# Kernel optimization log

Measured on AMD Instinct MI355X. Metric: run time of the kernel, lower is better.

## Reference

```python
import jax, jax.numpy as jnp
import numpy as np

BINS = 256
H = 2048
N = 2_000_000


def _tensor2image(x):
    # standard GAN denorm: [-1,1] -> [0,1]
    return (x + 1.0) * 0.5


def _cdf(vals):
    # torch.histc(bins=256, min=0, max=256): unit-width bins, values in [0,255]
    idx = jnp.clip(jnp.floor(vals), 0, BINS - 1).astype(jnp.int32)
    hist = jnp.zeros((BINS,), jnp.float32).at[idx].add(1.0)
    return jnp.cumsum(hist) / hist.sum()


def _trans_table(ref_cdf, adj_cdf):
    # cal_trans: for i in 1..255, first j in 1..255 with adj[j-1] <= ref[i] <= adj[j]
    i_vals = ref_cdf[1:]  # [255]
    cond = (adj_cdf[:-1][None, :] <= i_vals[:, None]) & (i_vals[:, None] <= adj_cdf[1:][None, :])  # [255,255]
    found = cond.any(axis=1)
    first_j = jnp.argmax(cond, axis=1) + 1
    tab = jnp.where(found, first_j, jnp.arange(1, BINS))  # unmatched entries keep identity
    tab = jnp.concatenate([jnp.zeros((1,), tab.dtype), tab])
    tab = tab.at[BINS - 1].set(BINS - 1)
    return tab.astype(jnp.float32)


def _hist_match(dst_img, ref_img, i0, i1, i2, i3):
    # dst_img, ref_img: [3,H,W]; indices: [N]
    dst_align = dst_img[:, i0, i1]  # [3,N]
    ref_align = ref_img[:, i2, i3]  # [3,N]
    cdf_dst = jax.vmap(_cdf)(dst_align)  # [3,256]
    cdf_ref = jax.vmap(_cdf)(ref_align)  # [3,256]
    tables = jax.vmap(_trans_table)(cdf_dst, cdf_ref)  # [3,256]
    bins = jnp.clip(dst_align, 0, BINS - 1).astype(jnp.int32)  # int() truncation on [0,255]
    new_align = jnp.take_along_axis(tables, bins, axis=1)  # [3,N]
    return dst_img.at[:, i0, i1].set(new_align)


def reference(input_data, target_data, mask_src, mask_tar, index0, index1, index2, index3, ref_data):
    inp = _tensor2image(input_data) * 255.0
    tgt = _tensor2image(target_data) * 255.0
    ref = _tensor2image(ref_data) * 255.0
    h = mask_src.shape[2]
    m_src = jnp.broadcast_to(mask_src, (1, 3, h, h))
    m_tar = jnp.broadcast_to(mask_tar, (1, 3, h, h))
    input_masked = inp * m_src
    target_masked = (tgt * m_tar)[0]  # [3,H,W]
    ref_masked = (ref * m_src)[0]     # [3,H,W]
    i0, i1, i2, i3 = index0[0], index1[0], index2[0], index3[0]
    matched = _hist_match(ref_masked, target_masked, i0, i1, i2, i3)[None]  # [1,3,H,W]
    input_match = jax.lax.stop_gradient(matched) * m_src  # no_grad in original
    return jnp.mean((input_masked - input_match) ** 2)


def setup_inputs() -> dict:
    key = jax.random.key(0)
    ks = jax.random.split(key, 9)
    inp = {
        "input_data": jax.random.uniform(ks[0], (1, 3, H, H), jnp.float32, -1.0, 1.0),
        "target_data": jax.random.uniform(ks[1], (1, 3, H, H), jnp.float32, -1.0, 1.0),
        "mask_src": (jax.random.uniform(ks[2], (1, 1, H, H)) > 0.5).astype(jnp.float32),
        "mask_tar": (jax.random.uniform(ks[3], (1, 1, H, H)) > 0.5).astype(jnp.float32),
        "index0": jax.random.randint(ks[4], (1, N), 0, H, jnp.int32),
        "index1": jax.random.randint(ks[5], (1, N), 0, H, jnp.int32),
        "index2": jax.random.randint(ks[6], (1, N), 0, H, jnp.int32),
        "index3": jax.random.randint(ks[7], (1, N), 0, H, jnp.int32),
        "ref_data": jax.random.uniform(ks[8], (1, 3, H, H), jnp.float32, -1.0, 1.0),
    }
    return inp
```

## Files before the change

kernel.cpp:

```cpp
#include <hip/hip_runtime.h>

#define HDIM 2048
#define HH (HDIM * HDIM)
#define NIDX 2000000
#define BINS 256
#define NCOPY 16
#define TL_BLOCKS 2048

#define PART_OFF     0
#define HIST_OFF     20480
#define BITS_OFF     131072
#define PACKED_D_OFF 1048576
#define PACKED_R_OFF 17825792

__global__ __launch_bounds__(256) void pack_kernel(
    const float* __restrict__ ref, const float* __restrict__ tgt,
    const float* __restrict__ msrc, const float* __restrict__ mtar,
    unsigned* __restrict__ packed_d, unsigned* __restrict__ packed_r,
    unsigned* __restrict__ hist, unsigned* __restrict__ bits)
{
    const int gtid = blockIdx.x * 256 + threadIdx.x;
    const int stride = gridDim.x * 256;

    for (int k = gtid; k < NCOPY * 6 * BINS; k += stride) hist[k] = 0;
    for (int k = gtid; k < HH / 32; k += stride) bits[k] = 0;

    for (int g = gtid; g < HH / 4; g += stride) {
        const int p = g * 4;
        const float4 ms4 = *(const float4*)(msrc + p);
        const float4 mt4 = *(const float4*)(mtar + p);
        const float ms[4] = {ms4.x, ms4.y, ms4.z, ms4.w};
        const float mt[4] = {mt4.x, mt4.y, mt4.z, mt4.w};
        unsigned od[4] = {0, 0, 0, 0}, orr[4] = {0, 0, 0, 0};
#pragma unroll
        for (int c = 0; c < 3; c++) {
            const float4 rv = *(const float4*)(ref + c * HH + p);
            const float4 tv = *(const float4*)(tgt + c * HH + p);
            const float r[4] = {rv.x, rv.y, rv.z, rv.w};
            const float tt[4] = {tv.x, tv.y, tv.z, tv.w};
#pragma unroll
            for (int k = 0; k < 4; k++) {
                const float vd = ((r[k] + 1.0f) * 0.5f) * 255.0f * ms[k];
                const float vr = ((tt[k] + 1.0f) * 0.5f) * 255.0f * mt[k];
                const unsigned bd = (unsigned)(int)fminf(fmaxf(floorf(vd), 0.0f), 255.0f);
                const unsigned br = (unsigned)(int)fminf(fmaxf(floorf(vr), 0.0f), 255.0f);
                od[k]  |= bd << (8 * c);
                orr[k] |= br << (8 * c);
            }
        }
        *(uint4*)(packed_d + p) = make_uint4(od[0], od[1], od[2], od[3]);
        *(uint4*)(packed_r + p) = make_uint4(orr[0], orr[1], orr[2], orr[3]);
    }
}

__global__ __launch_bounds__(256) void hist_kernel(
    const unsigned* __restrict__ packed_d, const unsigned* __restrict__ packed_r,
    const int* __restrict__ i0, const int* __restrict__ i1,
    const int* __restrict__ i2, const int* __restrict__ i3,
    unsigned* __restrict__ hist, unsigned* __restrict__ bits)
{
    __shared__ unsigned lhist[6 * BINS];
    for (int k = threadIdx.x; k < 6 * BINS; k += 256) lhist[k] = 0;
    __syncthreads();

    const int stride = gridDim.x * 256;
    for (int q = blockIdx.x * 256 + threadIdx.x; q < NIDX / 4; q += stride) {
        const int4 a = ((const int4*)i0)[q];
        const int4 b = ((const int4*)i1)[q];
        const int4 c = ((const int4*)i2)[q];
        const int4 d = ((const int4*)i3)[q];
        const int pd[4] = {a.x * HDIM + b.x, a.y * HDIM + b.y, a.z * HDIM + b.z, a.w * HDIM + b.w};
        const int pr[4] = {c.x * HDIM + d.x, c.y * HDIM + d.y, c.z * HDIM + d.z, c.w * HDIM + d.w};
        unsigned wd[4], wr[4];
#pragma unroll
        for (int k = 0; k < 4; k++) wd[k] = packed_d[pd[k]];
#pragma unroll
        for (int k = 0; k < 4; k++) wr[k] = packed_r[pr[k]];
#pragma unroll
        for (int k = 0; k < 4; k++) atomicOr(&bits[pd[k] >> 5], 1u << (pd[k] & 31));
#pragma unroll
        for (int k = 0; k < 4; k++) {
            atomicAdd(&lhist[           ( wd[k]        & 255u)], 1u);
            atomicAdd(&lhist[1 * BINS + ((wd[k] >> 8 ) & 255u)], 1u);
            atomicAdd(&lhist[2 * BINS + ((wd[k] >> 16) & 255u)], 1u);
            atomicAdd(&lhist[3 * BINS + ( wr[k]        & 255u)], 1u);
            atomicAdd(&lhist[4 * BINS + ((wr[k] >> 8 ) & 255u)], 1u);
            atomicAdd(&lhist[5 * BINS + ((wr[k] >> 16) & 255u)], 1u);
        }
    }
    __syncthreads();
    unsigned* h = hist + (blockIdx.x & (NCOPY - 1)) * (6 * BINS);
    for (int k = threadIdx.x; k < 6 * BINS; k += 256) {
        const unsigned v = lhist[k];
        if (v) atomicAdd(&h[k], v);
    }
}

__global__ __launch_bounds__(256) void tabloss_kernel(
    const float* __restrict__ inp, const float* __restrict__ ref,
    const float* __restrict__ msrc, const unsigned* __restrict__ hist,
    const unsigned* __restrict__ bits, double* __restrict__ partials)
{
    __shared__ float    cdf[6 * BINS];
    __shared__ float    tab[3 * BINS];
    __shared__ double   red[256];
    __shared__ unsigned wsum[4];

    const int t    = threadIdx.x;
    const int lane = t & 63;
    const int wid  = t >> 6;

    for (int ch = 0; ch < 6; ch++) {
        unsigned x = 0;
#pragma unroll
        for (int cp = 0; cp < NCOPY; cp++) x += hist[cp * (6 * BINS) + ch * BINS + t];
#pragma unroll
        for (int d = 1; d < 64; d <<= 1) {
            const unsigned y = __shfl_up(x, d, 64);
            if (lane >= d) x += y;
        }
        if (lane == 63) wsum[wid] = x;
        __syncthreads();
        unsigned prefix = 0;
        for (int w = 0; w < wid; w++) prefix += wsum[w];
        x += prefix;
        cdf[ch * BINS + t] = (float)x / 2000000.0f;
        __syncthreads();
    }
    for (int c = 0; c < 3; c++) {
        float o;
        if (t == 0)             o = 0.0f;
        else if (t == BINS - 1) o = 255.0f;
        else {
            const float v = cdf[c * BINS + t];
            const float* arr = cdf + (3 + c) * BINS;
            int lo = 0, hi = 256;
            while (lo < hi) { const int mid = (lo + hi) >> 1; if (arr[mid] < v) lo = mid + 1; else hi = mid; }
            const int J0 = ((lo > 1) ? lo : 1) - 1;
            int lo2 = 0, hi2 = 256;
            while (lo2 < hi2) { const int mid = (lo2 + hi2) >> 1; if (arr[mid] <= v) lo2 = mid + 1; else hi2 = mid; }
            const int J1 = ((lo2 - 1) < 254 ? (lo2 - 1) : 254);
            const bool found = (lo2 >= 1) && (J0 <= J1);
            o = found ? (float)(J0 + 1) : (float)t;
        }
        tab[c * BINS + t] = o;
    }
    __syncthreads();

    double local = 0.0;
    const int stride = gridDim.x * 256;
    for (int g = blockIdx.x * 256 + t; g < HH / 4; g += stride) {
        const int p = g * 4;
        const float4 mv = *(const float4*)(msrc + p);
        const unsigned w = bits[p >> 5] >> (p & 31);
        const float m[4] = {mv.x, mv.y, mv.z, mv.w};
#pragma unroll
        for (int c = 0; c < 3; c++) {
            const float4 rv = *(const float4*)(ref + c * HH + p);
            const float4 iv = *(const float4*)(inp + c * HH + p);
            const float r[4] = {rv.x, rv.y, rv.z, rv.w};
            const float x4[4] = {iv.x, iv.y, iv.z, iv.w};
            float s = 0.0f;
#pragma unroll
            for (int k = 0; k < 4; k++) {
                const float mm = m[k];
                const float refm = ((r[k] + 1.0f) * 0.5f) * 255.0f * mm;
                const float inpm = ((x4[k] + 1.0f) * 0.5f) * 255.0f * mm;
                float matchv;
                if ((w >> k) & 1u) {
                    const int bidx = (int)fminf(fmaxf(refm, 0.0f), 255.0f);
                    matchv = tab[c * BINS + bidx];
                } else {
                    matchv = refm;
                }
                const float dd = inpm - matchv * mm;
                s += dd * dd;
            }
            local += (double)s;
        }
    }
    red[t] = local;
    __syncthreads();
    for (int s2 = 128; s2 > 0; s2 >>= 1) {
        if (t < s2) red[t] += red[t + s2];
        __syncthreads();
    }
    if (t == 0) partials[blockIdx.x] = red[0];
}

__global__ __launch_bounds__(256) void finalize_kernel(
    const double* __restrict__ partials, float* __restrict__ out)
{
    const int t = threadIdx.x;
    double s = 0.0;
    for (int k = t; k < TL_BLOCKS; k += 256) s += partials[k];
    __shared__ double red[256];
    red[t] = s;
    __syncthreads();
    for (int s2 = 128; s2 > 0; s2 >>= 1) {
        if (t < s2) red[t] += red[t + s2];
        __syncthreads();
    }
    if (t == 0) out[0] = (float)(red[0] / (double)(3 * HH));
}

extern "C" void kernel_launch(void* const* d_in, const int* in_sizes, int n_in,
                              void* d_out, int out_size, void* d_ws, size_t ws_size,
                              hipStream_t stream)
{
    const float* input_data  = (const float*)d_in[0];
    const float* target_data = (const float*)d_in[1];
    const float* mask_src    = (const float*)d_in[2];
    const float* mask_tar    = (const float*)d_in[3];
    const int*   i0          = (const int*)d_in[4];
    const int*   i1          = (const int*)d_in[5];
    const int*   i2          = (const int*)d_in[6];
    const int*   i3          = (const int*)d_in[7];
    const float* ref_data    = (const float*)d_in[8];
    float* out = (float*)d_out;

    char* ws = (char*)d_ws;
    double*   partials = (double*)(ws + PART_OFF);
    unsigned* hist     = (unsigned*)(ws + HIST_OFF);
    unsigned* bits     = (unsigned*)(ws + BITS_OFF);
    unsigned* packed_d = (unsigned*)(ws + PACKED_D_OFF);
    unsigned* packed_r = (unsigned*)(ws + PACKED_R_OFF);

    pack_kernel<<<2048, 256, 0, stream>>>(ref_data, target_data, mask_src, mask_tar,
                                          packed_d, packed_r, hist, bits);
    hist_kernel<<<2048, 256, 0, stream>>>(packed_d, packed_r, i0, i1, i2, i3, hist, bits);
    tabloss_kernel<<<TL_BLOCKS, 256, 0, stream>>>(input_data, ref_data, mask_src, hist,
                                                  bits, partials);
    finalize_kernel<<<1, 256, 0, stream>>>(partials, out);
}
```

Before: 338.3 us.

## Bucket gather indices by address slice for L2-local histogram gathers

```diff
diff --git a/kernel.cpp b/kernel.cpp
--- a/kernel.cpp
+++ b/kernel.cpp
@@ -3,53 +3,139 @@
 #define HDIM 2048
 #define HH (HDIM * HDIM)
 #define NIDX 2000000
+#define QUADS (NIDX / 4)
 #define BINS 256
 #define NCOPY 16
 #define TL_BLOCKS 2048
 
+#define PACKB 2048
+#define BBLK 256
+#define QPB ((QUADS + BBLK - 1) / BBLK)
+#define NSLICE 8
+#define CAP 1152
+
 #define PART_OFF     0
 #define HIST_OFF     20480
 #define BITS_OFF     131072
+#define CNTS_OFF     655360
 #define PACKED_D_OFF 1048576
 #define PACKED_R_OFF 17825792
+#define BKT_PD_OFF   34603008
+#define BKT_PR_OFF   44040192
+#define WS_NEED      (BKT_PR_OFF + (size_t)BBLK * NSLICE * CAP * 4)
 
 __global__ __launch_bounds__(256) void pack_kernel(
     const float* __restrict__ ref, const float* __restrict__ tgt,
     const float* __restrict__ msrc, const float* __restrict__ mtar,
+    const int* __restrict__ i0, const int* __restrict__ i1,
+    const int* __restrict__ i2, const int* __restrict__ i3,
     unsigned* __restrict__ packed_d, unsigned* __restrict__ packed_r,
+    unsigned* __restrict__ hist, unsigned* __restrict__ bits,
+    unsigned* __restrict__ bkt_pd, unsigned* __restrict__ bkt_pr,
+    unsigned* __restrict__ cnts)
+{
+    const int t = threadIdx.x;
+    if (blockIdx.x < PACKB) {
+        const int gtid = blockIdx.x * 256 + t;
+        const int stride = PACKB * 256;
+
+        for (int k = gtid; k < NCOPY * 6 * BINS; k += stride) hist[k] = 0;
+        for (int k = gtid; k < HH / 32; k += stride) bits[k] = 0;
+
+        for (int g = gtid; g < HH / 4; g += stride) {
+            const int p = g * 4;
+            const float4 ms4 = *(const float4*)(msrc + p);
+            const float4 mt4 = *(const float4*)(mtar + p);
+            const float ms[4] = {ms4.x, ms4.y, ms4.z, ms4.w};
+            const float mt[4] = {mt4.x, mt4.y, mt4.z, mt4.w};
+            unsigned od[4] = {0, 0, 0, 0}, orr[4] = {0, 0, 0, 0};
+#pragma unroll
+            for (int c = 0; c < 3; c++) {
+                const float4 rv = *(const float4*)(ref + c * HH + p);
+                const float4 tv = *(const float4*)(tgt + c * HH + p);
+                const float r[4] = {rv.x, rv.y, rv.z, rv.w};
+                const float tt[4] = {tv.x, tv.y, tv.z, tv.w};
+#pragma unroll
+                for (int k = 0; k < 4; k++) {
+                    const float vd = ((r[k] + 1.0f) * 0.5f) * 255.0f * ms[k];
+                    const float vr = ((tt[k] + 1.0f) * 0.5f) * 255.0f * mt[k];
+                    const unsigned bd = (unsigned)(int)fminf(fmaxf(floorf(vd), 0.0f), 255.0f);
+                    const unsigned br = (unsigned)(int)fminf(fmaxf(floorf(vr), 0.0f), 255.0f);
+                    od[k]  |= bd << (8 * c);
+                    orr[k] |= br << (8 * c);
+                }
+            }
+            *(uint4*)(packed_d + p) = make_uint4(od[0], od[1], od[2], od[3]);
+            *(uint4*)(packed_r + p) = make_uint4(orr[0], orr[1], orr[2], orr[3]);
+        }
+    } else {
+        __shared__ unsigned lcur[2 * NSLICE];
+        if (t < 2 * NSLICE) lcur[t] = 0;
+        __syncthreads();
+
+        const int bb  = blockIdx.x - PACKB;
+        const int qlo = bb * QPB;
+        const int qhi = (qlo + QPB < QUADS) ? (qlo + QPB) : QUADS;
+        for (int q = qlo + t; q < qhi; q += 256) {
+            const int4 a = ((const int4*)i0)[q];
+            const int4 b = ((const int4*)i1)[q];
+            const int4 c = ((const int4*)i2)[q];
+            const int4 d = ((const int4*)i3)[q];
+            const int pd[4] = {a.x * HDIM + b.x, a.y * HDIM + b.y, a.z * HDIM + b.z, a.w * HDIM + b.w};
+            const int pr[4] = {c.x * HDIM + d.x, c.y * HDIM + d.y, c.z * HDIM + d.z, c.w * HDIM + d.w};
+#pragma unroll
+            for (int k = 0; k < 4; k++) {
+                const int sd = pd[k] >> 19;
+                const unsigned pos = atomicAdd(&lcur[sd], 1u);
+                if (pos < CAP) bkt_pd[(bb * NSLICE + sd) * CAP + pos] = (unsigned)pd[k];
+                const int sr = pr[k] >> 19;
+                const unsigned pos2 = atomicAdd(&lcur[NSLICE + sr], 1u);
+                if (pos2 < CAP) bkt_pr[(bb * NSLICE + sr) * CAP + pos2] = (unsigned)pr[k];
+            }
+        }
+        __syncthreads();
+        if (t < NSLICE) {
+            const unsigned v = lcur[t];
+            cnts[0 * BBLK * NSLICE + bb * NSLICE + t] = (v < CAP) ? v : CAP;
+        } else if (t < 2 * NSLICE) {
+            const unsigned v = lcur[t];
+            cnts[1 * BBLK * NSLICE + bb * NSLICE + (t - NSLICE)] = (v < CAP) ? v : CAP;
+        }
+    }
+}
+
+__global__ __launch_bounds__(256) void hist_bucket_kernel(
+    const unsigned* __restrict__ packed_d, const unsigned* __restrict__ packed_r,
+    const unsigned* __restrict__ bkt_pd, const unsigned* __restrict__ bkt_pr,
+    const unsigned* __restrict__ cnts,
     unsigned* __restrict__ hist, unsigned* __restrict__ bits)
 {
-    const int gtid = blockIdx.x * 256 + threadIdx.x;
-    const int stride = gridDim.x * 256;
-
-    for (int k = gtid; k < NCOPY * 6 * BINS; k += stride) hist[k] = 0;
-    for (int k = gtid; k < HH / 32; k += stride) bits[k] = 0;
-
-    for (int g = gtid; g < HH / 4; g += stride) {
-        const int p = g * 4;
-        const float4 ms4 = *(const float4*)(msrc + p);
-        const float4 mt4 = *(const float4*)(mtar + p);
-        const float ms[4] = {ms4.x, ms4.y, ms4.z, ms4.w};
-        const float mt[4] = {mt4.x, mt4.y, mt4.z, mt4.w};
-        unsigned od[4] = {0, 0, 0, 0}, orr[4] = {0, 0, 0, 0};
-#pragma unroll
-        for (int c = 0; c < 3; c++) {
-            const float4 rv = *(const float4*)(ref + c * HH + p);
-            const float4 tv = *(const float4*)(tgt + c * HH + p);
-            const float r[4] = {rv.x, rv.y, rv.z, rv.w};
-            const float tt[4] = {tv.x, tv.y, tv.z, tv.w};
-#pragma unroll
-            for (int k = 0; k < 4; k++) {
-                const float vd = ((r[k] + 1.0f) * 0.5f) * 255.0f * ms[k];
-                const float vr = ((tt[k] + 1.0f) * 0.5f) * 255.0f * mt[k];
-                const unsigned bd = (unsigned)(int)fminf(fmaxf(floorf(vd), 0.0f), 255.0f);
-                const unsigned br = (unsigned)(int)fminf(fmaxf(floorf(vr), 0.0f), 255.0f);
-                od[k]  |= bd << (8 * c);
-                orr[k] |= br << (8 * c);
-            }
-        }
-        *(uint4*)(packed_d + p) = make_uint4(od[0], od[1], od[2], od[3]);
-        *(uint4*)(packed_r + p) = make_uint4(orr[0], orr[1], orr[2], orr[3]);
+    __shared__ unsigned lhist[6 * BINS];
+    const int t = threadIdx.x;
+    for (int k = t; k < 6 * BINS; k += 256) lhist[k] = 0;
+    __syncthreads();
+
+    const int side = blockIdx.x >> 11;
+    const int s    = blockIdx.x & 7;
+    const int j    = (blockIdx.x & 2047) >> 3;
+    const unsigned cnt = cnts[side * BBLK * NSLICE + j * NSLICE + s];
+    const unsigned* bkt = (side ? bkt_pr : bkt_pd) + (j * NSLICE + s) * CAP;
+    const unsigned* packed = side ? packed_r : packed_d;
+    const int hbase = side ? 3 * BINS : 0;
+
+    for (unsigned i = t; i < cnt; i += 256) {
+        const unsigned p = bkt[i];
+        const unsigned w = packed[p];
+        if (!side) atomicOr(&bits[p >> 5], 1u << (p & 31));
+        atomicAdd(&lhist[hbase            + ( w        & 255u)], 1u);
+        atomicAdd(&lhist[hbase + 1 * BINS + ((w >> 8 ) & 255u)], 1u);
+        atomicAdd(&lhist[hbase + 2 * BINS + ((w >> 16) & 255u)], 1u);
+    }
+    __syncthreads();
+    unsigned* h = hist + (blockIdx.x & (NCOPY - 1)) * (6 * BINS);
+    for (int k = t; k < 3 * BINS; k += 256) {
+        const unsigned v = lhist[hbase + k];
+        if (v) atomicAdd(&h[hbase + k], v);
     }
 }
 
@@ -223,12 +309,26 @@
     double*   partials = (double*)(ws + PART_OFF);
     unsigned* hist     = (unsigned*)(ws + HIST_OFF);
     unsigned* bits     = (unsigned*)(ws + BITS_OFF);
+    unsigned* cnts     = (unsigned*)(ws + CNTS_OFF);
     unsigned* packed_d = (unsigned*)(ws + PACKED_D_OFF);
     unsigned* packed_r = (unsigned*)(ws + PACKED_R_OFF);
-
-    pack_kernel<<<2048, 256, 0, stream>>>(ref_data, target_data, mask_src, mask_tar,
-                                          packed_d, packed_r, hist, bits);
-    hist_kernel<<<2048, 256, 0, stream>>>(packed_d, packed_r, i0, i1, i2, i3, hist, bits);
+    unsigned* bkt_pd   = (unsigned*)(ws + BKT_PD_OFF);
+    unsigned* bkt_pr   = (unsigned*)(ws + BKT_PR_OFF);
+
+    const bool big_ws = (ws_size >= (size_t)WS_NEED);
+
+    if (big_ws) {
+        pack_kernel<<<PACKB + BBLK, 256, 0, stream>>>(
+            ref_data, target_data, mask_src, mask_tar, i0, i1, i2, i3,
+            packed_d, packed_r, hist, bits, bkt_pd, bkt_pr, cnts);
+        hist_bucket_kernel<<<4096, 256, 0, stream>>>(
+            packed_d, packed_r, bkt_pd, bkt_pr, cnts, hist, bits);
+    } else {
+        pack_kernel<<<PACKB, 256, 0, stream>>>(
+            ref_data, target_data, mask_src, mask_tar, i0, i1, i2, i3,
+            packed_d, packed_r, hist, bits, packed_d , packed_r , cnts);
+        hist_kernel<<<2048, 256, 0, stream>>>(packed_d, packed_r, i0, i1, i2, i3, hist, bits);
+    }
     tabloss_kernel<<<TL_BLOCKS, 256, 0, stream>>>(input_data, ref_data, mask_src, hist,
                                                   bits, partials);
     finalize_kernel<<<1, 256, 0, stream>>>(partials, out);
```

Measured after the change: 341.2 us. No clear change (+0.9%).
